# Kernel tuning notes

Hardware: AMD Instinct MI355X
Metric: run time of the kernel (lower is better)

The kernel has to match this reference:

```python
import jax, jax.numpy as jnp
import numpy as np

G = 8        # groups
GP = 16      # group_planes = out_planes // groups
A = 65       # adjusted_kernel (static: zero-init kernel_adjust -> sigmoid=0.5 -> eff=64 -> 65)
EDC = 10     # each_direction_channels (static: zero-init gamma_mapper -> c//12)
OFF = 2      # offset_step = min(max_dilation=2, min(h,w)//8)
EPS = 1e-5


def _rz(t, shape):
    # torch F.interpolate (align_corners=False, no antialias) == jax.image.resize linear, antialias=False
    return jax.image.resize(t, shape, method='linear', antialias=False)


def _bn(t, g, b, axis):
    # eval-mode BatchNorm with running_mean=0, running_var=1
    sh = [1] * t.ndim
    sh[axis] = -1
    return t * (g / jnp.sqrt(1.0 + EPS)).reshape(sh) + b.reshape(sh)


def setup_inputs() -> dict:
    key = jax.random.key(0)
    ks = jax.random.split(key, 5)
    N, C, H, W = 2, 128, 128, 128
    return {
        'x': jax.random.normal(ks[0], (N, C, H, W), jnp.float32),
        'w_qkv': jax.random.normal(ks[1], (2 * C, C), jnp.float32) * 0.05,
        'bn_qkv_g': jnp.ones((2 * C,), jnp.float32),
        'bn_qkv_b': jnp.zeros((2 * C,), jnp.float32),
        'bn_sim_g': jnp.ones((3 * G,), jnp.float32),
        'bn_sim_b': jnp.zeros((3 * G,), jnp.float32),
        'bn_out_g': jnp.ones((2 * C,), jnp.float32),
        'bn_out_b': jnp.zeros((2 * C,), jnp.float32),
        'in_w': jnp.ones((C,), jnp.float32),
        'in_b': jnp.zeros((C,), jnp.float32),
        'mlp_w1': jax.random.normal(ks[2], (4 * C, C), jnp.float32) * 0.05,
        'mlp_w2': jax.random.normal(ks[3], (C, 4 * C), jnp.float32) * 0.05,
        'base_relative': jax.random.normal(ks[4], (2 * GP, 255, 255), jnp.float32),
    }


def reference(x, w_qkv, bn_qkv_g, bn_qkv_b, bn_sim_g, bn_sim_b, bn_out_g, bn_out_b,
              in_w, in_b, mlp_w1, mlp_w2, base_relative):
    N, C, H, W = x.shape
    # ---- AdaptiveAxisAttention (width=False: attend along H) ----
    xp = jnp.transpose(x, (0, 3, 1, 2)).reshape(N * W, C, H)           # [NW,C,H]
    qkv = jnp.einsum('nci,oc->noi', xp, w_qkv)                          # 1x1 conv1d
    qkv = _bn(qkv, bn_qkv_g, bn_qkv_b, 1)
    qkv = qkv.reshape(N * W, G, 2 * GP, H)
    q, k, v = qkv[:, :, :GP // 2], qkv[:, :, GP // 2:GP], qkv[:, :, GP:]

    rel = _rz(base_relative, (2 * GP, A, A))                            # interp pos table
    q_emb, k_emb, v_emb = rel[:GP // 2], rel[GP // 2:GP], rel[GP:]

    # resize q,k,v along axis length H -> A (linear)
    qa = _rz(q, q.shape[:-1] + (A,))
    ka = _rz(k, k.shape[:-1] + (A,))
    va = _rz(v, v.shape[:-1] + (A,))

    qr = jnp.einsum('bgci,cij->bgij', qa, q_emb)
    kr = jnp.swapaxes(jnp.einsum('bgci,cij->bgij', ka, k_emb), 2, 3)
    qk = jnp.einsum('bgci,bgcj->bgij', qa, ka)
    stacked = jnp.concatenate([qk, qr, kr], axis=1)                     # [NW,3G,A,A]
    stacked = _bn(stacked, bn_sim_g, bn_sim_b, 1)
    sim = stacked.reshape(N * W, 3, G, A, A).sum(axis=1)                # [NW,G,A,A]
    sim = _rz(sim, (N * W, G, H, H))                                    # bilinear back to H
    sim = jax.nn.softmax(sim, axis=3)

    v_emb_h = _rz(v_emb, (GP, H, H))
    v_h = _rz(va, va.shape[:-1] + (H,))                                 # round-tripped v (A->H)

    sv = jnp.einsum('bgij,bgcj->bgci', sim, v_h)                        # [NW,G,GP,H]
    sve = jnp.einsum('bgij,cij->bgci', sim, v_emb_h)
    out = jnp.concatenate([sv, sve], axis=-1).reshape(N * W, 2 * C, H)
    out = _bn(out, bn_out_g, bn_out_b, 1)
    out = out.reshape(N, W, C, 2, H).sum(axis=3)                        # [N,W,C,H]
    y = jnp.transpose(out, (0, 2, 3, 1))                                # [N,C,H,W]

    # ---- AdaptiveSpatialBlock (static EDC/OFF; edge/gamma path only feeds .item(), no grad) ----
    identity = y
    s = y[:, :EDC]
    z = ((0, 0), (0, 0))
    right = jnp.pad(s[:, :, :, :-OFF], z + ((0, 0), (OFF, 0)))
    left = jnp.pad(s[:, :, :, OFF:], z + ((0, 0), (0, OFF)))
    down = jnp.pad(s[:, :, :-OFF, :], z + ((OFF, 0), (0, 0)))
    up = jnp.pad(s[:, :, OFF:, :], z + ((0, OFF), (0, 0)))
    xo = jnp.concatenate([right, left, down, up, y[:, 4 * EDC:]], axis=1)
    mu = xo.mean(axis=(2, 3), keepdims=True)
    var = xo.var(axis=(2, 3), keepdims=True)
    xn = (xo - mu) / jnp.sqrt(var + EPS) * in_w[None, :, None, None] + in_b[None, :, None, None]
    h1 = jax.nn.gelu(jnp.einsum('nchw,oc->nohw', xn, mlp_w1), approximate=False)
    h2 = jnp.einsum('nchw,oc->nohw', h1, mlp_w2)
    return h2 + identity
```

## Files before the change

### kernel.cpp

```cpp
#include <hip/hip_runtime.h>
#include <hip/hip_bf16.h>
#include <hip/hip_fp16.h>

#define GG 8
#define AA 65
#define BB 256

typedef __attribute__((ext_vector_type(8))) short bf16x8;
typedef __attribute__((ext_vector_type(4))) short s16x4;
typedef __attribute__((ext_vector_type(4))) float f32x4;
typedef _Float16 hf2 __attribute__((ext_vector_type(2)));
#define MFMA16(a, b, c) __builtin_amdgcn_mfma_f32_16x16x32_bf16(a, b, c, 0, 0, 0)
#define FDOT2(a, b, c) __builtin_amdgcn_fdot2((a), (b), (c), false)

__device__ __forceinline__ void rz_taps(int o, float scale, int in_size,
                                        int& ia, int& ib, float& f) {
  float pos = (o + 0.5f) * scale - 0.5f;
  float fl = floorf(pos);
  int i0 = (int)fl;
  f = pos - fl;
  ia = i0 < 0 ? 0 : i0;
  int i1 = i0 + 1;
  ib = i1 > (in_size - 1) ? (in_size - 1) : i1;
}

#define JTAP(jc, ja, jb, fj) \
  const int num_ = 130 * (jc) - 63;               \
  const int fl_ = num_ >> 8;                      \
  const int ja = fl_ < 0 ? 0 : fl_;               \
  const int jb = (fl_ + 1 > 64) ? 64 : (fl_ + 1); \
  const float fj = (float)(num_ - (fl_ << 8)) * 0.00390625f;

__device__ __forceinline__ float gelu_exact(float v) {
  return 0.5f * v * (1.0f + erff(v * 0.70710678118654752f));
}

__device__ __forceinline__ short f2b(float f) {
  __hip_bfloat16 h = __float2bfloat16(f);
  return *reinterpret_cast<short*>(&h);
}
__device__ __forceinline__ float b2f(short s) {
  unsigned int u = ((unsigned int)(unsigned short)s) << 16;
  return __uint_as_float(u);
}

#define RSBN 0.99999500003749977f

__global__ void k_prep(const float* __restrict__ base, const float* __restrict__ wq,
                       const float* __restrict__ w1, const float* __restrict__ w2,
                       short* __restrict__ wqb, short* __restrict__ w1b,
                       short* __restrict__ w2b, __half* __restrict__ relA2h,
                       __half* __restrict__ relAT2h, __half* __restrict__ veA4) {
  int blk = blockIdx.x;
  int tt = threadIdx.x;
  if (blk < 256) {
    int i = blk * 256 + tt;
    if (i < 32768) wqb[i] = f2b(wq[i]);
    w1b[i] = f2b(w1[i]);
    w2b[i] = f2b(w2[i]);
    return;
  }
  blk -= 256;
  if (blk < 265) {
    int idx = blk * 256 + tt;
    if (idx >= 16 * AA * AA) return;
    int j = idx % AA;
    int r = idx / AA;
    int i = r % AA;
    int c = r / AA;
    int ia, ib, ja, jb; float fi, fj;
    rz_taps(i, 255.0f / 65.0f, 255, ia, ib, fi);
    rz_taps(j, 255.0f / 65.0f, 255, ja, jb, fj);
    const float* S = base + (size_t)c * 255 * 255;
    float v = (1.0f - fi) * ((1.0f - fj) * S[ia * 255 + ja] + fj * S[ia * 255 + jb])
            + fi * ((1.0f - fj) * S[ib * 255 + ja] + fj * S[ib * 255 + jb]);
    if (c < 8) {
      relA2h[((((c >> 1) * 4420) + i * 68 + j) << 1) + (c & 1)] = __float2half(v);
    } else {
      int c2 = c - 8;
      relAT2h[((((c2 >> 1) * 4420) + j * 68 + i) << 1) + (c2 & 1)] = __float2half(v);
    }
    return;
  }
  blk -= 265;
  {
    int idx = blk * 256 + tt;
    if (idx >= 16 * 72 * 128) return;
    int i = idx & 127;
    int r = idx >> 7;
    int a = r % 72, c = r / 72;
    float v = 0.f;
    if (a < 65) {
      int ia, ib; float fi;
      rz_taps(i, 65.0f / 128.0f, 65, ia, ib, fi);
      int ja, jb; float fj;
      rz_taps(a, 255.0f / 65.0f, 255, ja, jb, fj);
      int p0a, p0b; float g0;
      rz_taps(ia, 255.0f / 65.0f, 255, p0a, p0b, g0);
      int p1a, p1b; float g1;
      rz_taps(ib, 255.0f / 65.0f, 255, p1a, p1b, g1);
      const float* S = base + (size_t)(16 + c) * 255 * 255;
      float r0 = (1.0f - g0) * ((1.0f - fj) * S[p0a * 255 + ja] + fj * S[p0a * 255 + jb])
               + g0 * ((1.0f - fj) * S[p0b * 255 + ja] + fj * S[p0b * 255 + jb]);
      float r1 = (1.0f - g1) * ((1.0f - fj) * S[p1a * 255 + ja] + fj * S[p1a * 255 + jb])
               + g1 * ((1.0f - fj) * S[p1b * 255 + ja] + fj * S[p1b * 255 + jb]);
      v = (1.0f - fi) * r0 + fi * r1;
    }
    veA4[(((size_t)(c * 9 + (a >> 3)) * 128 + i) << 3) + (a & 7)] = __float2half(v);
  }
}

__global__ __launch_bounds__(256) void k_qkv_mfma(
    const float* __restrict__ x, const short* __restrict__ wqb,
    const float* __restrict__ bg, const float* __restrict__ bb,
    short* __restrict__ out) {
  const int ob = blockIdx.x * 128;
  const int ya = blockIdx.y;
  const int a = ya >> 1;
  const int pb = (ya & 1) * 64;
  const int n = blockIdx.z;
  __shared__ short Asm[128 * 40];
  __shared__ short Bsm[64 * 40];
  const int t = threadIdx.x;
  const int lane = t & 63, wv = t >> 6;
  const int wm = wv >> 1, wn = wv & 1;
  const int lr = lane & 15, lk = (lane >> 4) * 8;
  int ia, ib; float f;
  rz_taps(a, 128.0f / 65.0f, 128, ia, ib, f);
  const float f0 = 1.0f - f;
  f32x4 acc[4][2];
  #pragma unroll
  for (int i = 0; i < 4; ++i)
    #pragma unroll
    for (int j = 0; j < 2; ++j)
      #pragma unroll
      for (int q = 0; q < 4; ++q) acc[i][j][q] = 0.f;
  const float* X = x + (size_t)n * 128 * 16384;
  for (int k0 = 0; k0 < 128; k0 += 32) {
    #pragma unroll
    for (int i2 = 0; i2 < 2; ++i2) {
      int u = t + 256 * i2;
      int row = u >> 2, kq = (u & 3) * 8;
      *(bf16x8*)&Asm[row * 40 + kq] = *(const bf16x8*)&wqb[(ob + row) * 128 + k0 + kq];
    }
    {
      int k = t >> 3, p8 = (t & 7) * 8;
      int c = k0 + k;
      const float* rowA = X + ((size_t)c * 128 + ia) * 128 + pb + p8;
      const float* rowB = X + ((size_t)c * 128 + ib) * 128 + pb + p8;
      float4 a0 = *(const float4*)rowA;
      float4 a1 = *(const float4*)(rowA + 4);
      float4 b0 = *(const float4*)rowB;
      float4 b1 = *(const float4*)(rowB + 4);
      short* d = &Bsm[p8 * 40 + k];
      d[0 * 40] = f2b(f0 * a0.x + f * b0.x);
      d[1 * 40] = f2b(f0 * a0.y + f * b0.y);
      d[2 * 40] = f2b(f0 * a0.z + f * b0.z);
      d[3 * 40] = f2b(f0 * a0.w + f * b0.w);
      d[4 * 40] = f2b(f0 * a1.x + f * b1.x);
      d[5 * 40] = f2b(f0 * a1.y + f * b1.y);
      d[6 * 40] = f2b(f0 * a1.z + f * b1.z);
      d[7 * 40] = f2b(f0 * a1.w + f * b1.w);
    }
    __syncthreads();
    bf16x8 af[4], bfr[2];
    #pragma unroll
    for (int mf = 0; mf < 4; ++mf) af[mf] = *(bf16x8*)&Asm[(wm * 64 + mf * 16 + lr) * 40 + lk];
    #pragma unroll
    for (int nf = 0; nf < 2; ++nf) bfr[nf] = *(bf16x8*)&Bsm[(wn * 32 + nf * 16 + lr) * 40 + lk];
    #pragma unroll
    for (int mf = 0; mf < 4; ++mf)
      #pragma unroll
      for (int nf = 0; nf < 2; ++nf)
        acc[mf][nf] = MFMA16(af[mf], bfr[nf], acc[mf][nf]);
    __syncthreads();
  }
  #pragma unroll
  for (int mf = 0; mf < 4; ++mf) {
    #pragma unroll
    for (int r = 0; r < 4; ++r) {
      int o = ob + wm * 64 + mf * 16 + (lane >> 4) * 4 + r;
      float sc = bg[o] * RSBN, sh = bb[o];
      #pragma unroll
      for (int nf = 0; nf < 2; ++nf) {
        int p = pb + wn * 32 + nf * 16 + lr;
        out[((size_t)(n * 256 + o) * 65 + a) * 128 + p] = f2b(acc[mf][nf][r] * sc + sh);
      }
    }
  }
}

__global__ void k_attn(const short* __restrict__ qkva, const __half* __restrict__ relA2,
                       const __half* __restrict__ relAT2, const __half* __restrict__ veA4,
                       const float* __restrict__ sg, const float* __restrict__ sb,
                       const float* __restrict__ og, const float* __restrict__ ob,
                       float* __restrict__ yT) {
  int orig = blockIdx.x;
  int bg = ((orig & 7) << 8) + (orig >> 3);
  int b = bg >> 3, g = bg & 7;
  int n = b >> 7, w = b & 127;
  __shared__ __attribute__((aligned(16))) float Ss[65 * 68];
  __shared__ __attribute__((aligned(16))) float u0[576];
  __half* PwsH = (__half*)Ss;
  float* Pinv2 = Ss + 4224;
  hf2* qs2 = (hf2*)u0;
  hf2* ks2v = (hf2*)(u0 + 260);
  float* ks2f = u0 + 260;
  __half* vasH = (__half*)u0;
  int t = threadIdx.x;
  const short* Qbase = qkva + ((size_t)(n * 256 + g * 32) * 65) * 128 + w;

  for (int l = t; l < 520; l += 256) {
    int isQ = (l < 260);
    int u2 = isQ ? l : l - 260;
    int cp = u2 / 65, a = u2 - cp * 65;
    int cbase = (cp << 1) + (isQ ? 0 : 8);
    float v0 = b2f(Qbase[(size_t)(cbase * 65 + a) * 128]);
    float v1 = b2f(Qbase[(size_t)((cbase + 1) * 65 + a) * 128]);
    hf2 h;
    h[0] = (_Float16)v0;
    h[1] = (_Float16)v1;
    if (isQ) qs2[cp * 65 + a] = h;
    else ks2v[cp * 68 + a] = h;
  }
  __syncthreads();

  {
    float sqk = sg[g] * RSBN, sqr = sg[8 + g] * RSBN, skr = sg[16 + g] * RSBN;
    float badd = sb[g] + sb[8 + g] + sb[16 + g];
    const float* rAf = (const float*)relA2;
    const float* rTf = (const float*)relAT2;
    const hf2* rAv = (const hf2*)relA2;
    const hf2* rTv = (const hf2*)relAT2;
    for (int u = t; u < 65 * 17; u += 256) {
      int i = u / 17, jq = u - i * 17;
      hf2 q2[4];
      #pragma unroll
      for (int cp = 0; cp < 4; ++cp) q2[cp] = qs2[cp * 65 + i];
      if (jq < 16) {
        int j0 = jq * 4;
        int lofs = i * 68 + j0;
        float qk0 = 0, qk1 = 0, qk2 = 0, qk3 = 0;
        float qr0 = 0, qr1 = 0, qr2 = 0, qr3 = 0;
        float kr0 = 0, kr1 = 0, kr2 = 0, kr3 = 0;
        #pragma unroll
        for (int cp = 0; cp < 4; ++cp) {
          float4 kq = *(const float4*)&ks2f[cp * 68 + j0];
          float4 ra = *(const float4*)&rAf[cp * 4420 + lofs];
          float4 rt = *(const float4*)&rTf[cp * 4420 + lofs];
          hf2 k0 = __builtin_bit_cast(hf2, kq.x);
          hf2 k1 = __builtin_bit_cast(hf2, kq.y);
          hf2 k2h = __builtin_bit_cast(hf2, kq.z);
          hf2 k3 = __builtin_bit_cast(hf2, kq.w);
          qk0 = FDOT2(k0, q2[cp], qk0);
          qk1 = FDOT2(k1, q2[cp], qk1);
          qk2 = FDOT2(k2h, q2[cp], qk2);
          qk3 = FDOT2(k3, q2[cp], qk3);
          qr0 = FDOT2(__builtin_bit_cast(hf2, ra.x), q2[cp], qr0);
          qr1 = FDOT2(__builtin_bit_cast(hf2, ra.y), q2[cp], qr1);
          qr2 = FDOT2(__builtin_bit_cast(hf2, ra.z), q2[cp], qr2);
          qr3 = FDOT2(__builtin_bit_cast(hf2, ra.w), q2[cp], qr3);
          kr0 = FDOT2(__builtin_bit_cast(hf2, rt.x), k0, kr0);
          kr1 = FDOT2(__builtin_bit_cast(hf2, rt.y), k1, kr1);
          kr2 = FDOT2(__builtin_bit_cast(hf2, rt.z), k2h, kr2);
          kr3 = FDOT2(__builtin_bit_cast(hf2, rt.w), k3, kr3);
        }
        float4 res;
        res.x = sqk * qk0 + sqr * qr0 + skr * kr0 + badd;
        res.y = sqk * qk1 + sqr * qr1 + skr * kr1 + badd;
        res.z = sqk * qk2 + sqr * qr2 + skr * kr2 + badd;
        res.w = sqk * qk3 + sqr * qr3 + skr * kr3 + badd;
        *(float4*)&Ss[lofs] = res;
      } else {
        int lofs = i * 68 + 64;
        float qk = 0, qr = 0, kr = 0;
        #pragma unroll
        for (int cp = 0; cp < 4; ++cp) {
          hf2 kv = ks2v[cp * 68 + 64];
          qk = FDOT2(kv, q2[cp], qk);
          qr = FDOT2(rAv[cp * 4420 + lofs], q2[cp], qr);
          kr = FDOT2(rTv[cp * 4420 + lofs], kv, kr);
        }
        Ss[lofs] = sqk * qk + sqr * qr + skr * kr + badd;
      }
    }
  }
  __syncthreads();

  for (int l = t; l < 16 * 72; l += 256) {
    int c = l / 72, a = l - c * 72;
    float v = (a < 65) ? b2f(Qbase[(size_t)((16 + c) * 65 + a) * 128]) : 0.f;
    vasH[l] = __float2half(v);
  }
  {
    const int i = t >> 1, h = t & 1;
    int ia, ib; float fi;
    rz_taps(i, 65.0f / 128.0f, 65, ia, ib, fi);
    const float* r0 = Ss + ia * 68 + h * 32;
    const float* r1 = Ss + ib * 68 + h * 32;
    const float wi0 = 1.0f - fi;
    float T[33];
    #pragma unroll
    for (int k4 = 0; k4 < 8; ++k4) {
      float4 a4 = *(const float4*)(r0 + 4 * k4);
      float4 b4 = *(const float4*)(r1 + 4 * k4);
      T[4 * k4 + 0] = wi0 * a4.x + fi * b4.x;
      T[4 * k4 + 1] = wi0 * a4.y + fi * b4.y;
      T[4 * k4 + 2] = wi0 * a4.z + fi * b4.z;
      T[4 * k4 + 3] = wi0 * a4.w + fi * b4.w;
    }
    T[32] = wi0 * r0[32] + fi * r1[32];
    float mx = T[0];
    #pragma unroll
    for (int k = 1; k < 33; ++k) mx = fmaxf(mx, T[k]);
    mx = fmaxf(mx, __shfl_xor(mx, 1));
    float p[33];
    #pragma unroll
    for (int k = 0; k < 33; ++k) p[k] = 0.f;
    float sum = 0.f;
    if (h == 0) {
      #pragma unroll
      for (int j = 0; j < 64; ++j) {
        JTAP(j, ja, jb, fj);
        float v = (1.0f - fj) * T[ja] + fj * T[jb];
        float e = __expf(v - mx);
        sum += e;
        p[ja] += e * (1.0f - fj);
        p[jb] += e * fj;
      }
    } else {
      #pragma unroll
      for (int j = 64; j < 128; ++j) {
        JTAP(j, ja, jb, fj);
        float v = (1.0f - fj) * T[ja - 32] + fj * T[jb - 32];
        float e = __expf(v - mx);
        sum += e;
        p[ja - 32] += e * (1.0f - fj);
        p[jb - 32] += e * fj;
      }
    }
    sum += __shfl_xor(sum, 1);
    float other = __shfl_xor(h ? p[0] : p[32], 1);
    __syncthreads();
    __half* prow = &PwsH[i * 66];
    if (h == 0) {
      p[32] += other;
      #pragma unroll
      for (int k = 0; k < 33; ++k) prow[k] = __float2half(p[k]);
      Pinv2[i] = 1.0f / sum;
    } else {
      p[0] += other;
      #pragma unroll
      for (int k = 0; k < 33; ++k) prow[32 + k] = __float2half(p[k]);
      prow[65] = __float2half(0.f);
    }
  }
  __syncthreads();

  {
    const int i = t & 127;
    const int cg = t >> 7;
    const float inv = Pinv2[i];
    hf2 pw[33];
    const hf2* prow2 = (const hf2*)&PwsH[i * 66];
    #pragma unroll
    for (int ap = 0; ap < 33; ++ap) pw[ap] = prow2[ap];
    #pragma unroll
    for (int l = 0; l < 8; ++l) {
      const int c = cg * 8 + l;
      const float4* vr4 = (const float4*)&vasH[c * 72];
      const float4* vp4 = (const float4*)veA4 + (size_t)(c * 9) * 128 + i;
      float sv0 = 0.f, sv1 = 0.f, se0 = 0.f, se1 = 0.f;
      #pragma unroll
      for (int q4 = 0; q4 < 8; ++q4) {
        float4 a4 = vr4[q4];
        float4 b4 = vp4[(size_t)q4 * 128];
        sv0 = FDOT2(__builtin_bit_cast(hf2, a4.x), pw[4 * q4 + 0], sv0);
        sv1 = FDOT2(__builtin_bit_cast(hf2, a4.y), pw[4 * q4 + 1], sv1);
        sv0 = FDOT2(__builtin_bit_cast(hf2, a4.z), pw[4 * q4 + 2], sv0);
        sv1 = FDOT2(__builtin_bit_cast(hf2, a4.w), pw[4 * q4 + 3], sv1);
        se0 = FDOT2(__builtin_bit_cast(hf2, b4.x), pw[4 * q4 + 0], se0);
        se1 = FDOT2(__builtin_bit_cast(hf2, b4.y), pw[4 * q4 + 1], se1);
        se0 = FDOT2(__builtin_bit_cast(hf2, b4.z), pw[4 * q4 + 2], se0);
        se1 = FDOT2(__builtin_bit_cast(hf2, b4.w), pw[4 * q4 + 3], se1);
      }
      {
        float4 a4 = vr4[8];
        float4 b4 = vp4[(size_t)8 * 128];
        sv0 = FDOT2(__builtin_bit_cast(hf2, a4.x), pw[32], sv0);
        se0 = FDOT2(__builtin_bit_cast(hf2, b4.x), pw[32], se0);
      }
      float sv = sv0 + sv1, se = se0 + se1;
      int c2 = g * 16 + c;
      int o0 = 2 * c2;
      float val = og[o0] * RSBN * (sv * inv) + ob[o0]
                + og[o0 + 1] * RSBN * (se * inv) + ob[o0 + 1];
      yT[((size_t)(n * 128 + c2)) * 16384 + w * 128 + i] = val;
    }
  }
}

__global__ __launch_bounds__(256) void k_xs(const float* __restrict__ yT,
                                            const float* __restrict__ inw,
                                            const float* __restrict__ inb,
                                            short* __restrict__ xnb,
                                            float* __restrict__ yStd) {
  int gid = blockIdx.x;
  int n, cs, cx = -1;
  bool wStd;
  if (gid < 256) {
    n = gid >> 7; cx = gid & 127;
    cs = (cx < 40) ? (cx % 10) : cx;
    wStd = (cx < 10) || (cx >= 40);
  } else {
    int u = gid - 256;
    n = u / 30; cs = 10 + (u % 30);
    wStd = true;
  }
  int dh = 0, dw = 0;
  if (cx >= 0) {
    if (cx < 10)       dw = -2;
    else if (cx < 20)  dw = 2;
    else if (cx < 30)  dh = -2;
    else if (cx < 40)  dh = 2;
  }
  __shared__ float Sb[128 * 130];
  __shared__ float sm[8];
  const float* src = yT + ((size_t)(n * 128 + cs)) * 16384;
  int t = threadIdx.x;
  #pragma unroll
  for (int l = 0; l < 16; ++l) {
    int q = t + l * 256;
    float4 v = *(const float4*)&src[q * 4];
    int w = q >> 5, i0 = (q * 4) & 127;
    float* d = &Sb[w * 130 + i0];
    *(float2*)d = make_float2(v.x, v.y);
    *(float2*)(d + 2) = make_float2(v.z, v.w);
  }
  __syncthreads();
  if (wStd) {
    float* dst = yStd + ((size_t)(n * 128 + cs)) * 16384;
    for (int l = 0; l < 64; ++l) {
      int idx = t + l * 256;
      int h = idx >> 7, w = idx & 127;
      dst[idx] = Sb[w * 130 + h];
    }
  }
  if (cx >= 0) {
    float s = 0.f, q2 = 0.f;
    for (int l = 0; l < 64; ++l) {
      int idx = t + l * 256;
      int h = idx >> 7, w = idx & 127;
      int hs = h + dh, ws = w + dw;
      float v = (hs >= 0 && hs < 128 && ws >= 0 && ws < 128) ? Sb[ws * 130 + hs] : 0.f;
      s += v; q2 += v * v;
    }
    #pragma unroll
    for (int o = 32; o; o >>= 1) { s += __shfl_down(s, o); q2 += __shfl_down(q2, o); }
    if ((t & 63) == 0) { sm[(t >> 6) * 2] = s; sm[(t >> 6) * 2 + 1] = q2; }
    __syncthreads();
    float S_ = sm[0] + sm[2] + sm[4] + sm[6];
    float Q_ = sm[1] + sm[3] + sm[5] + sm[7];
    float mean = S_ * (1.0f / 16384.0f);
    float var = Q_ * (1.0f / 16384.0f) - mean * mean;
    float scale = inw[cx] * rsqrtf(var + 1e-5f);
    float shift = inb[cx] - mean * scale;
    short* dst = xnb + ((size_t)(n * 128 + cx)) * 16384;
    for (int l = 0; l < 64; ++l) {
      int idx = t + l * 256;
      int h = idx >> 7, w = idx & 127;
      int hs = h + dh, ws = w + dw;
      float v = (hs >= 0 && hs < 128 && ws >= 0 && ws < 128) ? Sb[ws * 130 + hs] : 0.f;
      dst[idx] = f2b(v * scale + shift);
    }
  }
}

__global__ __launch_bounds__(256) void k_mlp(
    const short* __restrict__ xnb, const short* __restrict__ w1b,
    const short* __restrict__ w2b, const float* __restrict__ y,
    float* __restrict__ out) {
  const int pb = blockIdx.x * 32;
  const int n = blockIdx.z;
  __shared__ short Asm[128 * 40];
  __shared__ short Bxn[32 * 136];
  __shared__ short h1s[32 * 136];
  const int t = threadIdx.x;
  const int lane = t & 63, wv = t >> 6;
  const int wm = wv >> 1, wn = wv & 1;
  const int lr = lane & 15, lk = (lane >> 4) * 8;
  const short* X = xnb + (size_t)n * 128 * 16384;
  #pragma unroll
  for (int i2 = 0; i2 < 2; ++i2) {
    int u = t + 256 * i2;
    int c = u >> 2, p0 = (u & 3) * 8;
    bf16x8 hv = *(const bf16x8*)&X[(size_t)c * 16384 + pb + p0];
    #pragma unroll
    for (int j = 0; j < 8; ++j) Bxn[(p0 + j) * 136 + c] = hv[j];
  }
  f32x4 acc2[4][1];
  #pragma unroll
  for (int i = 0; i < 4; ++i)
    #pragma unroll
    for (int q = 0; q < 4; ++q) acc2[i][0][q] = 0.f;
  __syncthreads();

  for (int och = 0; och < 4; ++och) {
    f32x4 acc1[4][1];
    #pragma unroll
    for (int i = 0; i < 4; ++i)
      #pragma unroll
      for (int q = 0; q < 4; ++q) acc1[i][0][q] = 0.f;
    for (int c0 = 0; c0 < 128; c0 += 32) {
      #pragma unroll
      for (int i2 = 0; i2 < 2; ++i2) {
        int u = t + 256 * i2;
        int row = u >> 2, kq = (u & 3) * 8;
        *(bf16x8*)&Asm[row * 40 + kq] =
            *(const bf16x8*)&w1b[(och * 128 + row) * 128 + c0 + kq];
      }
      __syncthreads();
      bf16x8 af[4], bfr;
      #pragma unroll
      for (int mf = 0; mf < 4; ++mf)
        af[mf] = *(bf16x8*)&Asm[(wm * 64 + mf * 16 + lr) * 40 + lk];
      bfr = *(bf16x8*)&Bxn[(wn * 16 + lr) * 136 + c0 + lk];
      #pragma unroll
      for (int mf = 0; mf < 4; ++mf)
        acc1[mf][0] = MFMA16(af[mf], bfr, acc1[mf][0]);
      __syncthreads();
    }
    #pragma unroll
    for (int mf = 0; mf < 4; ++mf)
      #pragma unroll
      for (int r = 0; r < 4; ++r) {
        int o = wm * 64 + mf * 16 + (lane >> 4) * 4 + r;
        int p = wn * 16 + lr;
        h1s[p * 136 + o] = f2b(gelu_exact(acc1[mf][0][r]));
      }
    for (int k0 = 0; k0 < 128; k0 += 32) {
      #pragma unroll
      for (int i2 = 0; i2 < 2; ++i2) {
        int u = t + 256 * i2;
        int row = u >> 2, kq = (u & 3) * 8;
        *(bf16x8*)&Asm[row * 40 + kq] =
            *(const bf16x8*)&w2b[row * 512 + och * 128 + k0 + kq];
      }
      __syncthreads();
      bf16x8 af[4], bfr;
      #pragma unroll
      for (int mf = 0; mf < 4; ++mf)
        af[mf] = *(bf16x8*)&Asm[(wm * 64 + mf * 16 + lr) * 40 + lk];
      bfr = *(bf16x8*)&h1s[(wn * 16 + lr) * 136 + k0 + lk];
      #pragma unroll
      for (int mf = 0; mf < 4; ++mf)
        acc2[mf][0] = MFMA16(af[mf], bfr, acc2[mf][0]);
      __syncthreads();
    }
  }
  #pragma unroll
  for (int mf = 0; mf < 4; ++mf)
    #pragma unroll
    for (int r = 0; r < 4; ++r) {
      int o = wm * 64 + mf * 16 + (lane >> 4) * 4 + r;
      int p = pb + wn * 16 + lr;
      size_t base = ((size_t)(n * 128 + o)) * 16384 + p;
      out[base] = acc2[mf][0][r] + y[base];
    }
}

extern "C" void kernel_launch(void* const* d_in, const int* in_sizes, int n_in,
                              void* d_out, int out_size, void* d_ws, size_t ws_size,
                              hipStream_t stream) {
  const float* x        = (const float*)d_in[0];
  const float* w_qkv    = (const float*)d_in[1];
  const float* bn_qkv_g = (const float*)d_in[2];
  const float* bn_qkv_b = (const float*)d_in[3];
  const float* bn_sim_g = (const float*)d_in[4];
  const float* bn_sim_b = (const float*)d_in[5];
  const float* bn_out_g = (const float*)d_in[6];
  const float* bn_out_b = (const float*)d_in[7];
  const float* in_w     = (const float*)d_in[8];
  const float* in_b     = (const float*)d_in[9];
  const float* mlp_w1   = (const float*)d_in[10];
  const float* mlp_w2   = (const float*)d_in[11];
  const float* base_rel = (const float*)d_in[12];
  float* Wp = (float*)d_ws;

  __half* relA2  = (__half*)(Wp + 0);
  __half* relAT2 = (__half*)(Wp + 17680);
  __half* veA4   = (__half*)(Wp + 35360);
  float* yT      = Wp + 109088;
  float* yStd    = Wp + 4303392;
  short* wqb     = (short*)(Wp + 8497696);
  short* w1b     = (short*)(Wp + 8514080);
  short* w2b     = (short*)(Wp + 8546848);
  short* xnb     = (short*)(Wp + 8579616);
  short* qkva    = (short*)(Wp + 10676768);

  k_prep<<<dim3(1097), dim3(256), 0, stream>>>(base_rel, w_qkv, mlp_w1, mlp_w2,
                                               wqb, w1b, w2b, relA2, relAT2, veA4);
  k_qkv_mfma<<<dim3(2, 130, 2), dim3(256), 0, stream>>>(x, wqb, bn_qkv_g, bn_qkv_b, qkva);
  k_attn<<<dim3(2048), dim3(256), 0, stream>>>(qkva, relA2, relAT2, veA4,
                                               bn_sim_g, bn_sim_b, bn_out_g, bn_out_b, yT);
  k_xs<<<dim3(316), dim3(256), 0, stream>>>(yT, in_w, in_b, xnb, yStd);
  k_mlp<<<dim3(512, 1, 2), dim3(256), 0, stream>>>(xnb, w1b, w2b, yStd, (float*)d_out);
}
```

Before: 122.9 us.

## Store QKV in per-(n,g,w) contiguous layout for vectorized attention loads

The QKV projection kernel now stages its output tile in shared memory and writes it transposed so that each (batch, group, column) owns a contiguous block of 65x32 bf16 values. The attention kernel then reads its q/k/v inputs with 16-byte vector loads instead of scattered strided 2-byte gathers, and v gets a separate shared buffer so it loads in the same pass. This trades an extra LDS transpose and barrier in the producer for coalesced access in the consumer.

```diff
diff --git a/kernel.cpp b/kernel.cpp
--- a/kernel.cpp
+++ b/kernel.cpp
@@ -121,6 +121,7 @@
   const int n = blockIdx.z;
   __shared__ short Asm[128 * 40];
   __shared__ short Bsm[64 * 40];
+  __shared__ short Ct[128 * 65];
   const int t = threadIdx.x;
   const int lane = t & 63, wv = t >> 6;
   const int wm = wv >> 1, wn = wv & 1;
@@ -179,18 +180,32 @@
   for (int mf = 0; mf < 4; ++mf) {
     #pragma unroll
     for (int r = 0; r < 4; ++r) {
-      int o = ob + wm * 64 + mf * 16 + (lane >> 4) * 4 + r;
+      int ol = wm * 64 + mf * 16 + (lane >> 4) * 4 + r;
+      int o = ob + ol;
       float sc = bg[o] * RSBN, sh = bb[o];
       #pragma unroll
       for (int nf = 0; nf < 2; ++nf) {
-        int p = pb + wn * 32 + nf * 16 + lr;
-        out[((size_t)(n * 256 + o) * 65 + a) * 128 + p] = f2b(acc[mf][nf][r] * sc + sh);
-      }
-    }
-  }
-}
-
-__global__ void k_attn(const short* __restrict__ qkva, const __half* __restrict__ relA2,
+        int wl = wn * 32 + nf * 16 + lr;
+        Ct[ol * 65 + wl] = f2b(acc[mf][nf][r] * sc + sh);
+      }
+    }
+  }
+  __syncthreads();
+  {
+    int gi = wv, wl = lane;
+    int g = (ob >> 5) + gi;
+    short* dst = out + (((size_t)((n * 8 + g) * 128) + pb + wl) * 65 + a) * 32;
+    #pragma unroll
+    for (int h8 = 0; h8 < 4; ++h8) {
+      bf16x8 vv;
+      #pragma unroll
+      for (int e = 0; e < 8; ++e) vv[e] = Ct[(gi * 32 + h8 * 8 + e) * 65 + wl];
+      *(bf16x8*)(dst + h8 * 8) = vv;
+    }
+  }
+}
+
+__global__ void k_attn(const short* __restrict__ qkvT, const __half* __restrict__ relA2,
                        const __half* __restrict__ relAT2, const __half* __restrict__ veA4,
                        const float* __restrict__ sg, const float* __restrict__ sb,
                        const float* __restrict__ og, const float* __restrict__ ob,
@@ -200,28 +215,46 @@
   int b = bg >> 3, g = bg & 7;
   int n = b >> 7, w = b & 127;
   __shared__ __attribute__((aligned(16))) float Ss[65 * 68];
-  __shared__ __attribute__((aligned(16))) float u0[576];
+  __shared__ __attribute__((aligned(16))) float qkbuf[536];
+  __shared__ __attribute__((aligned(16))) __half vasH[16 * 72];
   __half* PwsH = (__half*)Ss;
   float* Pinv2 = Ss + 4224;
-  hf2* qs2 = (hf2*)u0;
-  hf2* ks2v = (hf2*)(u0 + 260);
-  float* ks2f = u0 + 260;
-  __half* vasH = (__half*)u0;
+  hf2* qs2 = (hf2*)qkbuf;
+  hf2* ks2v = (hf2*)(qkbuf + 260);
+  float* ks2f = qkbuf + 260;
   int t = threadIdx.x;
-  const short* Qbase = qkva + ((size_t)(n * 256 + g * 32) * 65) * 128 + w;
-
-  for (int l = t; l < 520; l += 256) {
-    int isQ = (l < 260);
-    int u2 = isQ ? l : l - 260;
-    int cp = u2 / 65, a = u2 - cp * 65;
-    int cbase = (cp << 1) + (isQ ? 0 : 8);
-    float v0 = b2f(Qbase[(size_t)(cbase * 65 + a) * 128]);
-    float v1 = b2f(Qbase[(size_t)((cbase + 1) * 65 + a) * 128]);
-    hf2 h;
-    h[0] = (_Float16)v0;
-    h[1] = (_Float16)v1;
-    if (isQ) qs2[cp * 65 + a] = h;
-    else ks2v[cp * 68 + a] = h;
+  const short* Qb = qkvT + (size_t)((n * 8 + g) * 128 + w) * 2080;
+
+  for (int l = t; l < 260; l += 256) {
+    bf16x8 raw = *(const bf16x8*)(Qb + l * 8);
+    int a = l >> 2;
+    int seg = l & 3;
+    if (seg == 0) {
+      #pragma unroll
+      for (int cp = 0; cp < 4; ++cp) {
+        hf2 h;
+        h[0] = (_Float16)b2f(raw[2 * cp]);
+        h[1] = (_Float16)b2f(raw[2 * cp + 1]);
+        qs2[cp * 65 + a] = h;
+      }
+    } else if (seg == 1) {
+      #pragma unroll
+      for (int cp = 0; cp < 4; ++cp) {
+        hf2 h;
+        h[0] = (_Float16)b2f(raw[2 * cp]);
+        h[1] = (_Float16)b2f(raw[2 * cp + 1]);
+        ks2v[cp * 68 + a] = h;
+      }
+    } else {
+      int c0 = (seg - 2) * 8;
+      #pragma unroll
+      for (int e = 0; e < 8; ++e)
+        vasH[(c0 + e) * 72 + a] = __float2half(b2f(raw[e]));
+    }
+  }
+  if (t < 112) {
+    int c = t / 7, ap = 65 + t % 7;
+    vasH[c * 72 + ap] = __float2half(0.f);
   }
   __syncthreads();
 
@@ -287,11 +320,6 @@
   }
   __syncthreads();
 
-  for (int l = t; l < 16 * 72; l += 256) {
-    int c = l / 72, a = l - c * 72;
-    float v = (a < 65) ? b2f(Qbase[(size_t)((16 + c) * 65 + a) * 128]) : 0.f;
-    vasH[l] = __float2half(v);
-  }
   {
     const int i = t >> 1, h = t & 1;
     int ia, ib; float fi;
@@ -596,12 +624,12 @@
   short* w1b     = (short*)(Wp + 8514080);
   short* w2b     = (short*)(Wp + 8546848);
   short* xnb     = (short*)(Wp + 8579616);
-  short* qkva    = (short*)(Wp + 10676768);
+  short* qkvT    = (short*)(Wp + 10676768);
 
   k_prep<<<dim3(1097), dim3(256), 0, stream>>>(base_rel, w_qkv, mlp_w1, mlp_w2,
                                                wqb, w1b, w2b, relA2, relAT2, veA4);
-  k_qkv_mfma<<<dim3(2, 130, 2), dim3(256), 0, stream>>>(x, wqb, bn_qkv_g, bn_qkv_b, qkva);
-  k_attn<<<dim3(2048), dim3(256), 0, stream>>>(qkva, relA2, relAT2, veA4,
+  k_qkv_mfma<<<dim3(2, 130, 2), dim3(256), 0, stream>>>(x, wqb, bn_qkv_g, bn_qkv_b, qkvT);
+  k_attn<<<dim3(2048), dim3(256), 0, stream>>>(qkvT, relA2, relAT2, veA4,
                                                bn_sim_g, bn_sim_b, bn_out_g, bn_out_b, yT);
   k_xs<<<dim3(316), dim3(256), 0, stream>>>(yT, in_w, in_b, xnb, yStd);
   k_mlp<<<dim3(512, 1, 2), dim3(256), 0, stream>>>(xnb, w1b, w2b, yStd, (float*)d_out);
```

New measurement: 114.6 us. 6.8% less time.
